# Optimization experiments

Measured on AMD Instinct MI355X. Metric: run time of the kernel, lower is better.

Reference implementation:

```python
import jax, jax.numpy as jnp
import numpy as np

B, T, C, H, HD = 2, 2048, 768, 12, 64


def setup_inputs() -> dict:
    key = jax.random.key(0)
    k0, k1, k2, k3 = jax.random.split(key, 4)
    x = jax.random.normal(k0, (B, T, C), dtype=jnp.float32)
    w_attn = jax.random.normal(k1, (3 * H * HD, C), dtype=jnp.float32) * 0.02
    b_attn = jnp.zeros((3 * H * HD,), dtype=jnp.float32)
    w_proj = jax.random.normal(k2, (C, H * HD), dtype=jnp.float32) * 0.02
    b_proj = jnp.zeros((C,), dtype=jnp.float32)
    sel_w = jax.random.normal(k3, (H,), dtype=jnp.float32) * 0.3
    return {"x": x, "w_attn": w_attn, "b_attn": b_attn,
            "w_proj": w_proj, "b_proj": b_proj, "sel_w": sel_w}


def reference(x, w_attn, b_attn, w_proj, b_proj, sel_w):
    Bc, Tc, Cc = x.shape
    Hc = sel_w.shape[0]
    HDc = w_attn.shape[0] // (3 * Hc)
    qkv = x @ w_attn.T + b_attn                          # [B,T,3*H*HD]
    q, k, v = jnp.split(qkv, 3, axis=2)
    q = q.reshape(Bc, Tc, Hc, HDc).transpose(0, 2, 1, 3)  # [B,H,T,HD]
    k = k.reshape(Bc, Tc, Hc, HDc).transpose(0, 2, 1, 3)
    v = v.reshape(Bc, Tc, Hc, HDc).transpose(0, 2, 1, 3)

    scale = 1.0 / np.sqrt(HDc).astype(np.float32)
    att = jnp.einsum('bhid,bhjd->bhij', q, k) * scale    # [B,H,T,T]
    causal = jnp.tril(jnp.ones((Tc, Tc), dtype=bool))
    neg_inf = jnp.asarray(-jnp.inf, dtype=att.dtype)
    att = jnp.where(causal[None, None], att, neg_inf)

    # selection head: per-head linear combo of (causally-zeroed) logits
    att0 = jnp.where(causal[None, None], att, 0.0)       # -inf -> 0 before combo
    S = jnp.einsum('bhij,h->bij', att0, sel_w)           # [B,T,T], bias=False
    S = jnp.where(causal[None], S, 0.0)
    S = jax.nn.relu(S)
    S = S.at[..., 0].set(0.0)                            # protect_bos_token
    S = S * (1.0 - jnp.eye(Tc, dtype=S.dtype))           # prevent_from_masking_myself

    FF = jnp.cumsum(S, axis=-2)                          # forgetting accumulation over rows
    FF_shifted = jnp.concatenate(
        [jnp.zeros_like(FF[..., :1, :]), FF[..., :-1, :]], axis=-2)

    att = jax.nn.softmax(att - FF_shifted[:, None], axis=-1)
    y = jnp.einsum('bhij,bhjd->bhid', att, v)            # [B,H,T,HD]
    y = y.transpose(0, 2, 1, 3).reshape(Bc, Tc, Hc * HDc)
    return y @ w_proj.T + b_proj
```

## Files before the change

kernel.cpp:

```cpp
#include <hip/hip_runtime.h>

#define B_   2
#define T_   2048
#define C_   768
#define H_   12
#define HD_  64
#define M_   (B_ * T_)
#define N3_  (3 * C_)
#define KB_  (C_ * 2)

typedef __bf16 bf16_t;
typedef bf16_t bf16x8 __attribute__((ext_vector_type(8)));
typedef float  floatx4 __attribute__((ext_vector_type(4)));

__device__ inline floatx4 mfma_bf16(bf16x8 a, bf16x8 b, floatx4 c) {
    return __builtin_amdgcn_mfma_f32_16x16x32_bf16(a, b, c, 0, 0, 0);
}

__device__ __forceinline__ void async_copy16(const void* g, void* l) {
    __builtin_amdgcn_global_load_lds(
        (const __attribute__((address_space(1))) void*)g,
        (__attribute__((address_space(3))) void*)l, 16, 0, 0);
}

__device__ __forceinline__ bf16x8 frag_read(const char* ldsbase, int row, int quad) {
    int slot = quad ^ ((row >> 1) & 3);
    return *(const bf16x8*)(ldsbase + row * 64 + slot * 16);
}

template<bool TRIPLE>
__device__ __forceinline__ void gemm_loop8(
    const char* Ah, const char* Al, const char* Bh, const char* Bl,
    char* lds, floatx4 (&acc)[4][2])
{
    int tid = threadIdx.x, lane = tid & 63, wave = tid >> 6;
    int l15 = lane & 15, quad = lane >> 4;
    int wr = wave >> 2, wc = wave & 3;
    const int PH = TRIPLE ? 32768 : 16384;
    auto stage1 = [&](const char* tile, char* base, int k0) {
        int p = tid;
        int r = p >> 2, slot = p & 3;
        int g = slot ^ ((r >> 1) & 3);
        async_copy16(tile + (size_t)r * KB_ + k0 + g * 16, base + p * 16);
    };
    auto stage = [&](int ph, int k0) {
        char* base = lds + ph * PH;
        stage1(Ah, base, k0);
        stage1(Bh, base + 8192, k0);
        if (TRIPLE) {
            stage1(Al, base + 16384, k0);
            stage1(Bl, base + 24576, k0);
        }
    };
    stage(0, 0);
    int ph = 0;
#pragma unroll 1
    for (int k0 = 0; k0 < KB_; k0 += 64) {
        __syncthreads();
        if (k0 + 64 < KB_) stage(ph ^ 1, k0 + 64);
        char* base = lds + ph * PH;
        bf16x8 ah[4], al[4], bh[2], bl[2];
#pragma unroll
        for (int t = 0; t < 4; ++t) {
            ah[t] = frag_read(base, wr * 64 + t * 16 + l15, quad);
            if (TRIPLE)
                al[t] = frag_read(base + 16384, wr * 64 + t * 16 + l15, quad);
        }
#pragma unroll
        for (int t = 0; t < 2; ++t) {
            bh[t] = frag_read(base + 8192, wc * 32 + t * 16 + l15, quad);
            if (TRIPLE)
                bl[t] = frag_read(base + 24576, wc * 32 + t * 16 + l15, quad);
        }
#pragma unroll
        for (int mi = 0; mi < 4; ++mi)
#pragma unroll
            for (int ni = 0; ni < 2; ++ni) {
                acc[mi][ni] = mfma_bf16(ah[mi], bh[ni], acc[mi][ni]);
                if (TRIPLE) {
                    acc[mi][ni] = mfma_bf16(ah[mi], bl[ni], acc[mi][ni]);
                    acc[mi][ni] = mfma_bf16(al[mi], bh[ni], acc[mi][ni]);
                }
            }
        ph ^= 1;
    }
}

__global__ __launch_bounds__(256) void prep_kernel(
    const float* __restrict__ x, const float* __restrict__ w_attn,
    const float* __restrict__ w_proj,
    bf16_t* __restrict__ x_hi, bf16_t* __restrict__ x_lo,
    bf16_t* __restrict__ w_hi, bf16_t* __restrict__ w_lo,
    bf16_t* __restrict__ wp_b, int nx, int nw, int np)
{
    int gid = blockIdx.x * 256 + threadIdx.x;
    if (gid < nx) {
        float f = x[gid];
        bf16_t h = (bf16_t)f;
        x_hi[gid] = h;
        x_lo[gid] = (bf16_t)(f - (float)h);
    } else if (gid < nx + nw) {
        int i = gid - nx;
        float f = w_attn[i];
        bf16_t h = (bf16_t)f;
        w_hi[i] = h;
        w_lo[i] = (bf16_t)(f - (float)h);
    } else if (gid < nx + nw + np) {
        int i = gid - nx - nw;
        wp_b[i] = (bf16_t)w_proj[i];
    }
}

__global__ __launch_bounds__(512) void qkv_gemm(
    const bf16_t* __restrict__ x_hi, const bf16_t* __restrict__ x_lo,
    const bf16_t* __restrict__ w_hi, const bf16_t* __restrict__ w_lo,
    const float* __restrict__ bias, const float* __restrict__ selw,
    bf16_t* __restrict__ q_hi, bf16_t* __restrict__ q_lo,
    bf16_t* __restrict__ kw_hi, bf16_t* __restrict__ kw_lo,
    bf16_t* __restrict__ k_b, bf16_t* __restrict__ v_b)
{
    extern __shared__ char lds[];
    int m0 = blockIdx.x * 128, n0 = blockIdx.y * 128;
    floatx4 acc[4][2];
#pragma unroll
    for (int i = 0; i < 4; ++i)
#pragma unroll
        for (int j = 0; j < 2; ++j) acc[i][j] = (floatx4){0.f, 0.f, 0.f, 0.f};
    if (n0 >= 2 * C_) {
        gemm_loop8<false>((const char*)(x_hi + (size_t)m0 * C_), nullptr,
                          (const char*)(w_hi + (size_t)n0 * C_), nullptr, lds, acc);
    } else {
        gemm_loop8<true>((const char*)(x_hi + (size_t)m0 * C_),
                         (const char*)(x_lo + (size_t)m0 * C_),
                         (const char*)(w_hi + (size_t)n0 * C_),
                         (const char*)(w_lo + (size_t)n0 * C_), lds, acc);
    }

    int tid = threadIdx.x, lane = tid & 63, wave = tid >> 6;
    int l15 = lane & 15, quad = lane >> 4;
    int wr = wave >> 2, wc = wave & 3;
    int cb = n0 + wc * 32;
#pragma unroll
    for (int ni = 0; ni < 2; ++ni) {
        int col = cb + ni * 16 + l15;
        float bb = bias[col];
#pragma unroll
        for (int mi = 0; mi < 4; ++mi)
#pragma unroll
            for (int r = 0; r < 4; ++r) {
                int row = m0 + wr * 64 + mi * 16 + quad * 4 + r;
                float v = acc[mi][ni][r] + bb;
                if (cb < C_) {
                    float vs = v * 0.125f;
                    bf16_t h = (bf16_t)vs;
                    q_hi[(size_t)row * C_ + col] = h;
                    q_lo[(size_t)row * C_ + col] = (bf16_t)(vs - (float)h);
                } else if (cb < 2 * C_) {
                    int c2 = col - C_;
                    k_b[(size_t)row * C_ + c2] = (bf16_t)v;
                    float kw = v * selw[c2 >> 6];
                    bf16_t h = (bf16_t)kw;
                    kw_hi[(size_t)row * C_ + c2] = h;
                    kw_lo[(size_t)row * C_ + c2] = (bf16_t)(kw - (float)h);
                } else {
                    v_b[(size_t)row * C_ + (col - 2 * C_)] = (bf16_t)v;
                }
            }
    }
}

#define SEG_    16
#define SEGLEN_ (T_ / SEG_)

__global__ __launch_bounds__(512) void s_gemm(
    const bf16_t* __restrict__ q_hi, const bf16_t* __restrict__ q_lo,
    const bf16_t* __restrict__ kw_hi, const bf16_t* __restrict__ kw_lo,
    float* __restrict__ SF, float* __restrict__ segsum)
{
    extern __shared__ char lds[];
    int t = blockIdx.x, b = blockIdx.z;
    int it = (int)((sqrtf(8.f * t + 1.f) - 1.f) * 0.5f);
    while ((it + 1) * (it + 2) / 2 <= t) ++it;
    while (it * (it + 1) / 2 > t) --it;
    int jt = t - it * (it + 1) / 2;
    int i0 = it * 128, j0 = jt * 128;
    float* out = SF + (size_t)b * T_ * T_;

    floatx4 acc[4][2];
#pragma unroll
    for (int i = 0; i < 4; ++i)
#pragma unroll
        for (int j = 0; j < 2; ++j) acc[i][j] = (floatx4){0.f, 0.f, 0.f, 0.f};
    size_t arow = ((size_t)b * T_ + i0) * C_;
    size_t brow = ((size_t)b * T_ + j0) * C_;
    gemm_loop8<true>((const char*)(q_hi + arow), (const char*)(q_lo + arow),
                     (const char*)(kw_hi + brow), (const char*)(kw_lo + brow),
                     lds, acc);

    int tid = threadIdx.x, lane = tid & 63, wave = tid >> 6;
    int l15 = lane & 15, quad = lane >> 4;
    int wr = wave >> 2, wc = wave & 3;
    float colsum[2] = {0.f, 0.f};
#pragma unroll
    for (int ni = 0; ni < 2; ++ni) {
        int j = j0 + wc * 32 + ni * 16 + l15;
#pragma unroll
        for (int mi = 0; mi < 4; ++mi)
#pragma unroll
            for (int r = 0; r < 4; ++r) {
                int i = i0 + wr * 64 + mi * 16 + quad * 4 + r;
                float s = acc[mi][ni][r];
                s = (j >= 1 && j < i) ? fmaxf(s, 0.f) : 0.f;
                out[(size_t)i * T_ + j] = s;
                colsum[ni] += s;
            }
    }
#pragma unroll
    for (int ni = 0; ni < 2; ++ni) {
        colsum[ni] += __shfl_xor(colsum[ni], 16);
        colsum[ni] += __shfl_xor(colsum[ni], 32);
    }
    float* red = (float*)lds;
    if (quad == 0) {
#pragma unroll
        for (int ni = 0; ni < 2; ++ni)
            red[wr * 128 + wc * 32 + ni * 16 + l15] = colsum[ni];
    }
    __syncthreads();
    if (tid < 128) {
        float ssum = red[tid] + red[128 + tid];
        segsum[((size_t)b * SEG_ + it) * T_ + j0 + tid] = ssum;
    }
}

__global__ __launch_bounds__(256) void scan_apply(
    float* __restrict__ SF, const float* __restrict__ segsum)
{
    int gid  = blockIdx.x * 256 + threadIdx.x;
    int j    = gid & (T_ - 1);
    int rest = gid >> 11;
    int seg  = rest & (SEG_ - 1);
    int b    = rest >> 4;
    if (seg * SEGLEN_ + SEGLEN_ - 1 < j) return;
    float run = 0.f;
    for (int s = 0; s < seg; ++s) {
        float v = (s * SEGLEN_ + SEGLEN_ - 1 <= j) ? 0.f
                : segsum[((size_t)b * SEG_ + s) * T_ + j];
        run += v;
    }
    float* col = SF + (size_t)b * T_ * T_ + (size_t)(seg * SEGLEN_) * T_ + j;
#pragma unroll 4
    for (int i = 0; i < SEGLEN_; ++i) {
        float s = col[(size_t)i * T_];
        s = (seg * SEGLEN_ + i > j) ? s : 0.f;
        col[(size_t)i * T_] = run;
        run += s;
    }
}

__global__ __launch_bounds__(256) void vt_kernel(
    const bf16_t* __restrict__ v_b, bf16_t* __restrict__ vt)
{
    __shared__ bf16_t tile[64][72];
    int t0 = blockIdx.x * 64, h = blockIdx.y, b = blockIdx.z;
    int tid = threadIdx.x;
    int r = tid >> 2, sl = tid & 3;
    const bf16_t* src = v_b + ((size_t)(b * T_ + t0 + r)) * C_ + h * HD_ + sl * 16;
    *(int4*)&tile[r][sl * 16]     = *(const int4*)src;
    *(int4*)&tile[r][sl * 16 + 8] = *(const int4*)(src + 8);
    __syncthreads();
    int hd = tid >> 2, q = tid & 3;
#pragma unroll
    for (int half = 0; half < 2; ++half) {
        int c0 = (q * 2 + half) * 8;
        union { int4 i4; bf16_t e[8]; } u;
#pragma unroll
        for (int kk = 0; kk < 8; ++kk) u.e[kk] = tile[c0 + kk][hd];
        *(int4*)(vt + ((size_t)(b * H_ + h) * HD_ + hd) * T_ + t0 + c0) = u.i4;
    }
}

__global__ __launch_bounds__(256) void attn_kernel(
    const bf16_t* __restrict__ q_b, const bf16_t* __restrict__ k_b,
    const bf16_t* __restrict__ vt_g, const float* __restrict__ FF,
    bf16_t* __restrict__ y_b)
{
    __shared__ __align__(16) char KL[2][8192];
    __shared__ __align__(16) char VL[2][8192];
    __shared__ __align__(16) float LS[4][16][68];

    int tid = threadIdx.x, lane = tid & 63, wave = tid >> 6;
    int l15 = lane & 15, quad = lane >> 4;
    int wzi = (int)blockIdx.y + 12 * (int)blockIdx.z;
    int bi  = (31 - (int)blockIdx.x + 11 * (wzi >> 3)) & 31;
    int h = blockIdx.y, b = blockIdx.z;
    int i0w = bi * 64 + wave * 16;
    int jmax = bi * 64 + 63;
    const floatx4 fzero = {0.f, 0.f, 0.f, 0.f};
    const float FM = 20.f;

    const bf16_t* qrow = q_b + ((size_t)b * T_ + i0w + l15) * C_ + h * HD_;
    bf16x8 qa0 = *(const bf16x8*)(qrow + quad * 8);
    bf16x8 qa1 = *(const bf16x8*)(qrow + 32 + quad * 8);

    const bf16_t* kbase = k_b + (size_t)b * T_ * C_ + h * HD_;
    const bf16_t* vbase = vt_g + (size_t)(b * H_ + h) * HD_ * T_;
    const float*  fp    = FF + ((size_t)b * T_ + i0w + l15) * T_ + quad * 8;

    auto stage = [&](int ph, int j0) {
#pragma unroll
        for (int i = 0; i < 2; ++i) {
            int p = (wave * 2 + i) * 64 + lane;
            int r = p >> 3, sp = p & 7, s = sp ^ (r & 7);
            async_copy16(kbase + (size_t)(j0 + r) * C_ + s * 8, &KL[ph][p * 16]);
        }
#pragma unroll
        for (int i = 0; i < 2; ++i) {
            int p = (wave * 2 + i) * 64 + lane;
            int r = p >> 3, sp = p & 7, s = sp ^ (r & 7);
            async_copy16(vbase + (size_t)r * T_ + j0 + s * 8, &VL[ph][p * 16]);
        }
    };

    float l_run = 0.f;
    floatx4 O[4];
#pragma unroll
    for (int nt = 0; nt < 4; ++nt) O[nt] = fzero;

    stage(0, 0);
    int ph = 0;
#pragma unroll 1
    for (int j0 = 0; j0 <= jmax; j0 += 64) {
        __syncthreads();
        if (j0 + 64 <= jmax) stage(ph ^ 1, j0 + 64);

        float ffv[16];
        *(floatx4*)&ffv[0]  = *(const floatx4*)(fp);
        *(floatx4*)&ffv[4]  = *(const floatx4*)(fp + 4);
        *(floatx4*)&ffv[8]  = *(const floatx4*)(fp + 32);
        *(floatx4*)&ffv[12] = *(const floatx4*)(fp + 36);
        fp += 64;

        floatx4 pc[4];
#pragma unroll
        for (int s = 0; s < 4; ++s) {
            int r = s * 16 + l15;
            bf16x8 k0 = *(const bf16x8*)&KL[ph][r * 128 + ((quad     ^ (r & 7)) * 16)];
            bf16x8 k1 = *(const bf16x8*)&KL[ph][r * 128 + (((quad+4) ^ (r & 7)) * 16)];
            floatx4 p = mfma_bf16(qa0, k0, fzero);
            pc[s] = mfma_bf16(qa1, k1, p);
        }
#pragma unroll
        for (int s = 0; s < 4; ++s)
#pragma unroll
            for (int r = 0; r < 4; ++r)
                LS[wave][quad * 4 + r][s * 16 + l15] = pc[s][r];
        float qk[16];
        *(floatx4*)&qk[0]  = *(const floatx4*)&LS[wave][l15][quad * 8];
        *(floatx4*)&qk[4]  = *(const floatx4*)&LS[wave][l15][quad * 8 + 4];
        *(floatx4*)&qk[8]  = *(const floatx4*)&LS[wave][l15][32 + quad * 8];
        *(floatx4*)&qk[12] = *(const floatx4*)&LS[wave][l15][32 + quad * 8 + 4];

        float lg[16];
#pragma unroll
        for (int c = 0; c < 16; ++c) lg[c] = qk[c] - ffv[c];
        if (j0 + 63 > i0w) {
            int i = i0w + l15;
#pragma unroll
            for (int c = 0; c < 16; ++c) {
                int j = j0 + (c >> 3) * 32 + quad * 8 + (c & 7);
                lg[c] = (j <= i) ? lg[c] : -__builtin_inff();
            }
        }
        float p[16], ps = 0.f;
#pragma unroll
        for (int c = 0; c < 16; ++c) { p[c] = __expf(lg[c] - FM); ps += p[c]; }
        ps += __shfl_xor(ps, 16);
        ps += __shfl_xor(ps, 32);
        l_run += ps;

        bf16x8 pa0, pa1;
#pragma unroll
        for (int c = 0; c < 8; ++c) { pa0[c] = (bf16_t)p[c]; pa1[c] = (bf16_t)p[8 + c]; }
#pragma unroll
        for (int nt = 0; nt < 4; ++nt) {
            int r = nt * 16 + l15;
            bf16x8 v0 = *(const bf16x8*)&VL[ph][r * 128 + ((quad     ^ (r & 7)) * 16)];
            bf16x8 v1 = *(const bf16x8*)&VL[ph][r * 128 + (((quad+4) ^ (r & 7)) * 16)];
            O[nt] = mfma_bf16(pa0, v0, O[nt]);
            O[nt] = mfma_bf16(pa1, v1, O[nt]);
        }
        ph ^= 1;
    }

#pragma unroll
    for (int r = 0; r < 4; ++r) {
        float inv = 1.f / __shfl(l_run, quad * 4 + r);
        int i = i0w + quad * 4 + r;
#pragma unroll
        for (int nt = 0; nt < 4; ++nt)
            y_b[((size_t)b * T_ + i) * C_ + h * HD_ + nt * 16 + l15] =
                (bf16_t)(O[nt][r] * inv);
    }
}

__global__ __launch_bounds__(512) void proj_gemm(
    const bf16_t* __restrict__ y_b, const bf16_t* __restrict__ wp_b,
    const float* __restrict__ bias, float* __restrict__ out)
{
    extern __shared__ char lds[];
    int m0 = blockIdx.x * 128, n0 = blockIdx.y * 128;
    floatx4 acc[4][2];
#pragma unroll
    for (int i = 0; i < 4; ++i)
#pragma unroll
        for (int j = 0; j < 2; ++j) acc[i][j] = (floatx4){0.f, 0.f, 0.f, 0.f};
    gemm_loop8<false>((const char*)(y_b + (size_t)m0 * C_), nullptr,
                      (const char*)(wp_b + (size_t)n0 * C_), nullptr, lds, acc);

    int tid = threadIdx.x, lane = tid & 63, wave = tid >> 6;
    int l15 = lane & 15, quad = lane >> 4;
    int wr = wave >> 2, wc = wave & 3;
#pragma unroll
    for (int ni = 0; ni < 2; ++ni) {
        int col = n0 + wc * 32 + ni * 16 + l15;
        float bb = bias[col];
#pragma unroll
        for (int mi = 0; mi < 4; ++mi)
#pragma unroll
            for (int r = 0; r < 4; ++r)
                out[(size_t)(m0 + wr * 64 + mi * 16 + quad * 4 + r) * C_ + col] =
                    acc[mi][ni][r] + bb;
    }
}

extern "C" void kernel_launch(void* const* d_in, const int* in_sizes, int n_in,
                              void* d_out, int out_size, void* d_ws, size_t ws_size,
                              hipStream_t stream)
{
    const float* x      = (const float*)d_in[0];
    const float* w_attn = (const float*)d_in[1];
    const float* b_attn = (const float*)d_in[2];
    const float* w_proj = (const float*)d_in[3];
    const float* b_proj = (const float*)d_in[4];
    const float* sel_w  = (const float*)d_in[5];
    float* out = (float*)d_out;

    char* ws = (char*)d_ws;
    size_t off = 0;
    auto alloc = [&](size_t bytes) {
        void* p = ws + off;
        off += (bytes + 255) & ~(size_t)255;
        return p;
    };
    const size_t MC2 = (size_t)M_ * C_ * 2;
    bf16_t* q_hi   = (bf16_t*)alloc(MC2);
    bf16_t* q_lo   = (bf16_t*)alloc(MC2);
    bf16_t* kw_hi  = (bf16_t*)alloc(MC2);
    bf16_t* kw_lo  = (bf16_t*)alloc(MC2);
    bf16_t* k_b    = (bf16_t*)alloc(MC2);
    bf16_t* v_b    = (bf16_t*)alloc(MC2);
    bf16_t* y_b    = (bf16_t*)alloc(MC2);
    bf16_t* wp_b   = (bf16_t*)alloc((size_t)C_ * C_ * 2);
    float*  segsum = (float*)alloc((size_t)B_ * SEG_ * T_ * 4);
    char* shared_base = (char*)alloc((size_t)B_ * T_ * T_ * 4);
    bf16_t* x_hi = (bf16_t*)shared_base;
    bf16_t* x_lo = (bf16_t*)(shared_base + MC2);
    bf16_t* w_hi = (bf16_t*)(shared_base + 2 * MC2);
    bf16_t* w_lo = (bf16_t*)(shared_base + 2 * MC2 + (size_t)N3_ * C_ * 2);
    float*  SF   = (float*)shared_base;
    bf16_t* vt   = kw_hi;

    int nx = M_ * C_, nw = N3_ * C_, np = C_ * C_;
    int ntot = nx + nw + np;
    prep_kernel<<<dim3((ntot + 255) / 256), 256, 0, stream>>>(
        x, w_attn, w_proj, x_hi, x_lo, w_hi, w_lo, wp_b, nx, nw, np);

    qkv_gemm<<<dim3(M_ / 128, N3_ / 128), 512, 65536, stream>>>(
        x_hi, x_lo, w_hi, w_lo, b_attn, sel_w,
        q_hi, q_lo, kw_hi, kw_lo, k_b, v_b);
    s_gemm<<<dim3(136, 1, B_), 512, 65536, stream>>>(
        q_hi, q_lo, kw_hi, kw_lo, SF, segsum);
    vt_kernel<<<dim3(T_ / 64, H_, B_), 256, 0, stream>>>(v_b, vt);
    scan_apply<<<dim3(B_ * SEG_ * T_ / 256), 256, 0, stream>>>(SF, segsum);
    attn_kernel<<<dim3(T_ / 64, H_, B_), 256, 0, stream>>>(q_hi, k_b, vt, SF, y_b);
    proj_gemm<<<dim3(M_ / 128, C_ / 128), 512, 32768, stream>>>(y_b, wp_b, b_proj, out);
}
```

Before: 257.0 us.

## Split long causal attention tiles across two blocks and merge partial outputs

The attention grid becomes 48 blocks per head. Row tiles 16-31 are split into two KV halves whose partial O and l sums go to scratch buffers, and a new merge kernel combines them. This balances the causal triangle so no block processes 32 KV chunks. The change also replaces the fp32 LDS transpose of scores with a direct bf16 P write into swizzled LDS, and computes softmax in the MFMA output layout with strided FF loads. The costs are an extra kernel launch, fp32 partial-output traffic, and scratch memory aliased onto buffers assumed dead by then.

```diff
diff --git a/kernel.cpp b/kernel.cpp
--- a/kernel.cpp
+++ b/kernel.cpp
@@ -283,21 +283,24 @@
 __global__ __launch_bounds__(256) void attn_kernel(
     const bf16_t* __restrict__ q_b, const bf16_t* __restrict__ k_b,
     const bf16_t* __restrict__ vt_g, const float* __restrict__ FF,
-    bf16_t* __restrict__ y_b)
+    bf16_t* __restrict__ y_b, float* __restrict__ opart,
+    float* __restrict__ lpart)
 {
     __shared__ __align__(16) char KL[2][8192];
     __shared__ __align__(16) char VL[2][8192];
-    __shared__ __align__(16) float LS[4][16][68];
+    __shared__ __align__(16) bf16_t PB[4][1024];
 
     int tid = threadIdx.x, lane = tid & 63, wave = tid >> 6;
     int l15 = lane & 15, quad = lane >> 4;
-    int wzi = (int)blockIdx.y + 12 * (int)blockIdx.z;
-    int bi  = (31 - (int)blockIdx.x + 11 * (wzi >> 3)) & 31;
+    int u = blockIdx.x & 15, g = blockIdx.x >> 4;
+    int tile, jlo, jhi, half;
+    bool split;
+    if (g == 0)      { tile = 16 + u; jlo = 0;  jhi = 15;       half = 0; split = true;  }
+    else if (g == 1) { tile = u;      jlo = 0;  jhi = u;        half = 0; split = false; }
+    else             { tile = 31 - u; jlo = 16; jhi = 31 - u;   half = 1; split = true;  }
     int h = blockIdx.y, b = blockIdx.z;
-    int i0w = bi * 64 + wave * 16;
-    int jmax = bi * 64 + 63;
+    int i0w = tile * 64 + wave * 16;
     const floatx4 fzero = {0.f, 0.f, 0.f, 0.f};
-    const float FM = 20.f;
 
     const bf16_t* qrow = q_b + ((size_t)b * T_ + i0w + l15) * C_ + h * HD_;
     bf16x8 qa0 = *(const bf16x8*)(qrow + quad * 8);
@@ -305,7 +308,10 @@
 
     const bf16_t* kbase = k_b + (size_t)b * T_ * C_ + h * HD_;
     const bf16_t* vbase = vt_g + (size_t)(b * H_ + h) * HD_ * T_;
-    const float*  fp    = FF + ((size_t)b * T_ + i0w + l15) * T_ + quad * 8;
+    const float* fpr[4];
+#pragma unroll
+    for (int r = 0; r < 4; ++r)
+        fpr[r] = FF + ((size_t)b * T_ + i0w + quad * 4 + r) * T_ + jlo * 64 + l15;
 
     auto stage = [&](int ph, int j0) {
 #pragma unroll
@@ -322,25 +328,25 @@
         }
     };
 
-    float l_run = 0.f;
+    float l_lane[4] = {0.f, 0.f, 0.f, 0.f};
     floatx4 O[4];
 #pragma unroll
     for (int nt = 0; nt < 4; ++nt) O[nt] = fzero;
 
-    stage(0, 0);
+    stage(0, jlo * 64);
     int ph = 0;
 #pragma unroll 1
-    for (int j0 = 0; j0 <= jmax; j0 += 64) {
+    for (int jc = jlo; jc <= jhi; ++jc) {
         __syncthreads();
-        if (j0 + 64 <= jmax) stage(ph ^ 1, j0 + 64);
-
-        float ffv[16];
-        *(floatx4*)&ffv[0]  = *(const floatx4*)(fp);
-        *(floatx4*)&ffv[4]  = *(const floatx4*)(fp + 4);
-        *(floatx4*)&ffv[8]  = *(const floatx4*)(fp + 32);
-        *(floatx4*)&ffv[12] = *(const floatx4*)(fp + 36);
-        fp += 64;
-
+        if (jc < jhi) stage(ph ^ 1, (jc + 1) * 64);
+
+        float ff[4][4];
+#pragma unroll
+        for (int r = 0; r < 4; ++r) {
+#pragma unroll
+            for (int s = 0; s < 4; ++s) ff[s][r] = fpr[r][s * 16];
+            fpr[r] += 64;
+        }
         floatx4 pc[4];
 #pragma unroll
         for (int s = 0; s < 4; ++s) {
@@ -350,38 +356,37 @@
             floatx4 p = mfma_bf16(qa0, k0, fzero);
             pc[s] = mfma_bf16(qa1, k1, p);
         }
+        bool diag = (jc * 64 + 63 > i0w);
+        float p[4][4];
 #pragma unroll
         for (int s = 0; s < 4; ++s)
 #pragma unroll
-            for (int r = 0; r < 4; ++r)
-                LS[wave][quad * 4 + r][s * 16 + l15] = pc[s][r];
-        float qk[16];
-        *(floatx4*)&qk[0]  = *(const floatx4*)&LS[wave][l15][quad * 8];
-        *(floatx4*)&qk[4]  = *(const floatx4*)&LS[wave][l15][quad * 8 + 4];
-        *(floatx4*)&qk[8]  = *(const floatx4*)&LS[wave][l15][32 + quad * 8];
-        *(floatx4*)&qk[12] = *(const floatx4*)&LS[wave][l15][32 + quad * 8 + 4];
-
-        float lg[16];
-#pragma unroll
-        for (int c = 0; c < 16; ++c) lg[c] = qk[c] - ffv[c];
-        if (j0 + 63 > i0w) {
-            int i = i0w + l15;
-#pragma unroll
-            for (int c = 0; c < 16; ++c) {
-                int j = j0 + (c >> 3) * 32 + quad * 8 + (c & 7);
-                lg[c] = (j <= i) ? lg[c] : -__builtin_inff();
+            for (int r = 0; r < 4; ++r) {
+                float lg = pc[s][r] - ff[s][r] - 20.f;
+                if (diag) {
+                    int i = i0w + quad * 4 + r;
+                    int j = jc * 64 + s * 16 + l15;
+                    lg = (j <= i) ? lg : -__builtin_inff();
+                }
+                p[s][r] = __expf(lg);
             }
-        }
-        float p[16], ps = 0.f;
-#pragma unroll
-        for (int c = 0; c < 16; ++c) { p[c] = __expf(lg[c] - FM); ps += p[c]; }
-        ps += __shfl_xor(ps, 16);
-        ps += __shfl_xor(ps, 32);
-        l_run += ps;
-
-        bf16x8 pa0, pa1;
-#pragma unroll
-        for (int c = 0; c < 8; ++c) { pa0[c] = (bf16_t)p[c]; pa1[c] = (bf16_t)p[8 + c]; }
+#pragma unroll
+        for (int r = 0; r < 4; ++r)
+            l_lane[r] += (p[0][r] + p[1][r]) + (p[2][r] + p[3][r]);
+
+        bf16_t* Pw = &PB[wave][0];
+#pragma unroll
+        for (int s = 0; s < 4; ++s)
+#pragma unroll
+            for (int r = 0; r < 4; ++r) {
+                int rr = quad * 4 + r;
+                int ch = (s * 2 + (l15 >> 3)) ^ (rr & 7);
+                Pw[rr * 64 + ch * 8 + (l15 & 7)] = (bf16_t)p[s][r];
+            }
+        asm volatile("s_waitcnt lgkmcnt(0)" ::: "memory");
+        int xk = l15 & 7;
+        bf16x8 pa0 = *(const bf16x8*)&Pw[l15 * 64 + ((quad ^ xk) * 8)];
+        bf16x8 pa1 = *(const bf16x8*)&Pw[l15 * 64 + (((4 + quad) ^ xk) * 8)];
 #pragma unroll
         for (int nt = 0; nt < 4; ++nt) {
             int r = nt * 16 + l15;
@@ -394,13 +399,54 @@
     }
 
 #pragma unroll
-    for (int r = 0; r < 4; ++r) {
-        float inv = 1.f / __shfl(l_run, quad * 4 + r);
-        int i = i0w + quad * 4 + r;
-#pragma unroll
-        for (int nt = 0; nt < 4; ++nt)
-            y_b[((size_t)b * T_ + i) * C_ + h * HD_ + nt * 16 + l15] =
-                (bf16_t)(O[nt][r] * inv);
+    for (int r = 0; r < 4; ++r)
+#pragma unroll
+        for (int d = 1; d < 16; d <<= 1)
+            l_lane[r] += __shfl_xor(l_lane[r], d);
+
+    if (!split) {
+#pragma unroll
+        for (int r = 0; r < 4; ++r) {
+            float inv = 1.f / l_lane[r];
+            int i = i0w + quad * 4 + r;
+#pragma unroll
+            for (int nt = 0; nt < 4; ++nt)
+                y_b[((size_t)b * T_ + i) * C_ + h * HD_ + nt * 16 + l15] =
+                    (bf16_t)(O[nt][r] * inv);
+        }
+    } else {
+        size_t ob = ((((size_t)(b * H_ + h) * 16 + (tile - 16)) * 2 + half) * 4096);
+#pragma unroll
+        for (int r = 0; r < 4; ++r) {
+            int rl = wave * 16 + quad * 4 + r;
+#pragma unroll
+            for (int nt = 0; nt < 4; ++nt)
+                opart[ob + (size_t)rl * 64 + nt * 16 + l15] = O[nt][r];
+        }
+        if (l15 == 0) {
+            size_t lb = (((size_t)(b * H_ + h) * 16 + (tile - 16)) * 2 + half) * 64;
+#pragma unroll
+            for (int r = 0; r < 4; ++r)
+                lpart[lb + wave * 16 + quad * 4 + r] = l_lane[r];
+        }
+    }
+}
+
+__global__ __launch_bounds__(256) void merge_kernel(
+    const float* __restrict__ opart, const float* __restrict__ lpart,
+    bf16_t* __restrict__ y_b)
+{
+    int tt = blockIdx.x, h = blockIdx.y, b = blockIdx.z;
+    size_t b0 = (((size_t)(b * H_ + h) * 16 + tt) * 2) * 4096;
+    size_t l0 = (((size_t)(b * H_ + h) * 16 + tt) * 2) * 64;
+    int tile = 16 + tt;
+#pragma unroll 4
+    for (int e = threadIdx.x; e < 4096; e += 256) {
+        int row = e >> 6, col = e & 63;
+        float l = lpart[l0 + row] + lpart[l0 + 64 + row];
+        float o = opart[b0 + e] + opart[b0 + 4096 + e];
+        y_b[((size_t)b * T_ + tile * 64 + row) * C_ + h * HD_ + col] =
+            (bf16_t)(o / l);
     }
 }
 
@@ -455,14 +501,17 @@
     };
     const size_t MC2 = (size_t)M_ * C_ * 2;
     bf16_t* q_hi   = (bf16_t*)alloc(MC2);
-    bf16_t* q_lo   = (bf16_t*)alloc(MC2);
     bf16_t* kw_hi  = (bf16_t*)alloc(MC2);
-    bf16_t* kw_lo  = (bf16_t*)alloc(MC2);
     bf16_t* k_b    = (bf16_t*)alloc(MC2);
-    bf16_t* v_b    = (bf16_t*)alloc(MC2);
     bf16_t* y_b    = (bf16_t*)alloc(MC2);
     bf16_t* wp_b   = (bf16_t*)alloc((size_t)C_ * C_ * 2);
     float*  segsum = (float*)alloc((size_t)B_ * SEG_ * T_ * 4);
+    char* dead_base = (char*)alloc(3 * MC2);
+    bf16_t* q_lo  = (bf16_t*)dead_base;
+    bf16_t* kw_lo = (bf16_t*)(dead_base + MC2);
+    bf16_t* v_b   = (bf16_t*)(dead_base + 2 * MC2);
+    float*  opart = (float*)dead_base;
+    float*  lpart = (float*)(dead_base + (size_t)B_ * H_ * 16 * 2 * 4096 * 4);
     char* shared_base = (char*)alloc((size_t)B_ * T_ * T_ * 4);
     bf16_t* x_hi = (bf16_t*)shared_base;
     bf16_t* x_lo = (bf16_t*)(shared_base + MC2);
@@ -483,6 +532,8 @@
         q_hi, q_lo, kw_hi, kw_lo, SF, segsum);
     vt_kernel<<<dim3(T_ / 64, H_, B_), 256, 0, stream>>>(v_b, vt);
     scan_apply<<<dim3(B_ * SEG_ * T_ / 256), 256, 0, stream>>>(SF, segsum);
-    attn_kernel<<<dim3(T_ / 64, H_, B_), 256, 0, stream>>>(q_hi, k_b, vt, SF, y_b);
+    attn_kernel<<<dim3(48, H_, B_), 256, 0, stream>>>(
+        q_hi, k_b, vt, SF, y_b, opart, lpart);
+    merge_kernel<<<dim3(16, H_, B_), 256, 0, stream>>>(opart, lpart, y_b);
     proj_gemm<<<dim3(M_ / 128, C_ / 128), 512, 32768, stream>>>(y_b, wp_b, b_proj, out);
 }
```

After: 254.9 us. Within noise of the previous version (-0.8%).
